# Kernel optimization log

Hardware: AMD Instinct MI355X
Metric: run time of the kernel (lower is better)

## Reference

```python
import jax, jax.numpy as jnp
import numpy as np
from jax import lax

DIM = 256
NUM_HEADS = 8
HEAD_DIM = DIM // NUM_HEADS
SCALE = HEAD_DIM ** -0.5


def _avg_pool(x, k, p):
    # torch AvgPool2d(kernel=k, stride=1, padding=p) with count_include_pad=True
    s = lax.reduce_window(x, 0.0, lax.add,
                          window_dimensions=(1, 1, k, k),
                          window_strides=(1, 1, 1, 1),
                          padding=((0, 0), (0, 0), (p, p), (p, p)))
    return s / (k * k)


def setup_inputs() -> dict:
    key = jax.random.key(0)
    ks = jax.random.split(key, 7)
    x = jax.random.normal(ks[0], (2, DIM, 48, 48), dtype=jnp.float32)
    q_w = jax.random.normal(ks[1], (DIM, DIM), dtype=jnp.float32) * (DIM ** -0.5)
    q_b = jax.random.normal(ks[2], (DIM,), dtype=jnp.float32) * 0.02
    kv_w = jax.random.normal(ks[3], (2 * DIM, DIM), dtype=jnp.float32) * (DIM ** -0.5)
    kv_b = jax.random.normal(ks[4], (2 * DIM,), dtype=jnp.float32) * 0.02
    proj_w = jax.random.normal(ks[5], (DIM, DIM), dtype=jnp.float32) * (DIM ** -0.5)
    proj_b = jax.random.normal(ks[6], (DIM,), dtype=jnp.float32) * 0.02
    return {"x": x, "q_w": q_w, "q_b": q_b, "kv_w": kv_w, "kv_b": kv_b,
            "proj_w": proj_w, "proj_b": proj_b}


def reference(x, q_w, q_b, kv_w, kv_b, proj_w, proj_b):
    B, C, H, W = x.shape
    h, d, N = NUM_HEADS, HEAD_DIM, H * W

    # q = 1x1 conv -> [B, h, N, d]
    q = jnp.einsum('oc,bchw->bohw', q_w, x) + q_b[None, :, None, None]
    q = q.reshape(B, h, d, N).transpose(0, 1, 3, 2)

    # kv is a linear 1x1 conv, so (kv(x)+kv(p1)+kv(p2)+kv(p3))/4 == kv(mean of inputs)
    x_avg = (x + _avg_pool(x, 3, 1) + _avg_pool(x, 5, 2) + _avg_pool(x, 7, 3)) / 4.0
    kv = jnp.einsum('oc,bchw->bohw', kv_w, x_avg) + kv_b[None, :, None, None]
    kv = kv.reshape(B, 2, h, d, N).transpose(1, 0, 2, 4, 3)  # [2, B, h, N, d]
    k, v = kv[0], kv[1]

    attn = jnp.einsum('bhnd,bhmd->bhnm', q, k) * SCALE  # [B, h, N, N]
    attn = jax.nn.softmax(attn, axis=-1)
    y = jnp.einsum('bhnm,bhmd->bhnd', attn, v)  # [B, h, N, d]
    # faithful to torch: transpose(1,2) then flat reshape to [B, C, H, W]
    y = y.transpose(0, 2, 1, 3).reshape(B, C, H, W)

    out = jnp.einsum('oc,bchw->bohw', proj_w, y) + proj_b[None, :, None, None]
    return out
```

## Files before the change

kernel.cpp:

```cpp
#include <hip/hip_runtime.h>
#include <hip/hip_bf16.h>
#include <cstdint>

#define DIMC  256
#define NH    8
#define HD    32
#define NPIX  2304
#define BATCH 2
#define KT    32
#define NT2   (NPIX / KT)

typedef short s16x8 __attribute__((ext_vector_type(8)));
typedef short s16x4 __attribute__((ext_vector_type(4)));
typedef float f32x4 __attribute__((ext_vector_type(4)));

#define MFMA32(A,B,C) __builtin_amdgcn_mfma_f32_16x16x32_bf16(A,B,C,0,0,0)

__device__ inline uint32_t rnau(float x) { return __float_as_uint(x) + 0x8000u; }
__device__ inline uint32_t pk2(uint32_t l_, uint32_t h_) {
  return __builtin_amdgcn_perm(h_, l_, 0x07060302u);
}

__global__ __launch_bounds__(256) void pool_kernel(const float* __restrict__ x,
                                                   float* __restrict__ xavg) {
  const int plane = blockIdx.x;
  const float* xp = x + (size_t)plane * NPIX;
  __shared__ float sx[NPIX];
  __shared__ float h3[NPIX], h5[NPIX], h7[NPIX];
  const int t = threadIdx.x;
#pragma unroll
  for (int r = 0; r < 9; ++r) sx[r * 256 + t] = xp[r * 256 + t];
  __syncthreads();
#pragma unroll
  for (int r = 0; r < 9; ++r) {
    int p = r * 256 + t;
    int i = p / 48, j = p - i * 48;
    float a3 = 0.f, a5 = 0.f, a7 = 0.f;
#pragma unroll
    for (int dj = -3; dj <= 3; ++dj) {
      int jj = j + dj;
      if (jj < 0 || jj >= 48) continue;
      float v = sx[i * 48 + jj];
      a7 += v;
      if (dj >= -2 && dj <= 2) a5 += v;
      if (dj >= -1 && dj <= 1) a3 += v;
    }
    h3[p] = a3; h5[p] = a5; h7[p] = a7;
  }
  __syncthreads();
#pragma unroll
  for (int r = 0; r < 9; ++r) {
    int p = r * 256 + t;
    int i = p / 48, j = p - i * 48;
    float b3 = 0.f, b5 = 0.f, b7 = 0.f;
#pragma unroll
    for (int di = -3; di <= 3; ++di) {
      int ii = i + di;
      if (ii < 0 || ii >= 48) continue;
      int q = ii * 48 + j;
      b7 += h7[q];
      if (di >= -2 && di <= 2) b5 += h5[q];
      if (di >= -1 && di <= 1) b3 += h3[q];
    }
    xavg[(size_t)plane * NPIX + p] =
        0.25f * (sx[p] + b3 * (1.f / 9.f) + b5 * (1.f / 25.f) + b7 * (1.f / 49.f));
  }
}

__global__ __launch_bounds__(256) void conv_all(
    const float* __restrict__ x, const float* __restrict__ xavg,
    const float* __restrict__ qw, const float* __restrict__ kvw,
    const float* __restrict__ pw_,
    short* __restrict__ Xh, short* __restrict__ Ah,
    short* __restrict__ Wth) {
  const int bx = blockIdx.x;
  const int t = threadIdx.x;
  if (bx < 576) {
    const float* src = (bx < 288) ? x : xavg;
    short* dhi = (bx < 288) ? Xh : Ah;
    const int bb = (bx < 288) ? bx : bx - 288;
    const int n0 = (bb % 36) * 64, c0 = ((bb / 36) & 3) * 64, b = bb / 144;
    __shared__ __align__(16) float T[64][68];
    {
      const int c = t >> 2, n4 = (t & 3) * 16;
      const float* sp = src + ((size_t)b * DIMC + c0 + c) * NPIX + n0 + n4;
#pragma unroll
      for (int i2 = 0; i2 < 4; ++i2)
        *(f32x4*)&T[c][n4 + i2 * 4] = *(const f32x4*)(sp + i2 * 4);
    }
    __syncthreads();
    {
      const int n = t >> 2, c4 = (t & 3) * 16;
      float v[16];
#pragma unroll
      for (int i = 0; i < 16; ++i) v[i] = T[c4 + i][n];
      uint32_t a[16];
#pragma unroll
      for (int i = 0; i < 16; ++i) a[i] = rnau(v[i]);
      union { s16x8 s; uint32_t u[4]; } H0, H1;
#pragma unroll
      for (int j = 0; j < 4; ++j) {
        H0.u[j] = pk2(a[2 * j], a[2 * j + 1]);
        H1.u[j] = pk2(a[8 + 2 * j], a[8 + 2 * j + 1]);
      }
      const size_t off = ((size_t)b * NPIX + n0 + n) * DIMC + c0 + c4;
      *(s16x8*)(dhi + off) = H0.s; *(s16x8*)(dhi + off + 8) = H1.s;
    }
  } else {
    const int idx = ((bx - 576) * 256 + t) * 8;
    const float* s;
    int off;
    if (idx < 65536)       { s = qw;  off = idx; }
    else if (idx < 196608) { s = kvw; off = idx - 65536; }
    else                   { s = pw_; off = idx - 196608; }
    f32x4 x0 = *(const f32x4*)(s + off);
    f32x4 x1 = *(const f32x4*)(s + off + 4);
    float v[8] = {x0[0], x0[1], x0[2], x0[3], x1[0], x1[1], x1[2], x1[3]};
    uint32_t a[8];
#pragma unroll
    for (int i = 0; i < 8; ++i) a[i] = rnau(v[i]);
    union { s16x8 s; uint32_t u[4]; } H;
#pragma unroll
    for (int j = 0; j < 4; ++j) H.u[j] = pk2(a[2 * j], a[2 * j + 1]);
    *(s16x8*)(Wth + idx) = H.s;
  }
}

__global__ __launch_bounds__(128) void gemm_qkv_hi(
    const short* __restrict__ Wth,
    const float* __restrict__ q_b, const float* __restrict__ kv_b,
    const short* __restrict__ Xh, const short* __restrict__ Ah,
    short* __restrict__ Qhi, short* __restrict__ Khi, short* __restrict__ Vhi,
    float qscale) {
  __shared__ __align__(16) float Cl[32][68];
  const int by = blockIdx.y;
  const bool isQ = (by < 8);
  const int o0 = isQ ? by * 32 : (by - 8) * 32;
  const short* Wh = isQ ? Wth : Wth + 65536;
  const float* bias = isQ ? q_b : kv_b;
  const short* Inh = isQ ? Xh : Ah;
  const float scale = isQ ? qscale : 1.0f;
  short* d1 = isQ ? Qhi : Khi;
  const int n0 = blockIdx.x * 64;
  const int b  = blockIdx.z;

  const int tid = threadIdx.x;
  const int wave = tid >> 6, lane = tid & 63;
  const int g = lane >> 4, q = lane & 15;

  const short* wph = Wh + ((o0 + wave * 16 + q) * DIMC + g * 8);
  const short* iph = Inh + ((size_t)(b * NPIX + n0 + q) * DIMC + g * 8);

  f32x4 acc[4] = {{0,0,0,0},{0,0,0,0},{0,0,0,0},{0,0,0,0}};
#pragma unroll
  for (int c0 = 0; c0 < DIMC; c0 += 32) {
    s16x8 ah = *(const s16x8*)(wph + c0);
#pragma unroll
    for (int st = 0; st < 4; ++st) {
      s16x8 bh_ = *(const s16x8*)(iph + (size_t)st * 16 * DIMC + c0);
      acc[st] = MFMA32(ah, bh_, acc[st]);
    }
  }
#pragma unroll
  for (int st = 0; st < 4; ++st)
#pragma unroll
    for (int r = 0; r < 4; ++r)
      Cl[wave * 16 + g * 4 + r][st * 16 + q] = acc[st][r];
  __syncthreads();

  if (o0 < 256) {
    const int n = tid >> 1, oq = tid & 1;
    const int h = o0 >> 5;
    const float* bp = bias + o0 + oq * 16;
    float v[16];
#pragma unroll
    for (int i = 0; i < 16; ++i) v[i] = (Cl[oq * 16 + i][n] + bp[i]) * scale;
    uint32_t a[16];
#pragma unroll
    for (int i = 0; i < 16; ++i) a[i] = rnau(v[i]);
    union { s16x8 s; uint32_t u[4]; } H0, H1;
#pragma unroll
    for (int j = 0; j < 4; ++j) {
      H0.u[j] = pk2(a[2 * j], a[2 * j + 1]);
      H1.u[j] = pk2(a[8 + 2 * j], a[8 + 2 * j + 1]);
    }
    const size_t off = ((size_t)((b * 8 + h) * NPIX + n0 + n)) * HD + oq * 16;
    *(s16x8*)(d1 + off) = H0.s; *(s16x8*)(d1 + off + 8) = H1.s;
  } else {
    const int o = tid >> 2, nc = (tid & 3) * 16;
    const int h = (o0 - 256) >> 5;
    const float bv = bias[o0 + o];
    float v[16];
#pragma unroll
    for (int i2 = 0; i2 < 4; ++i2) {
      f32x4 t4 = *(const f32x4*)&Cl[o][nc + i2 * 4];
      v[i2 * 4 + 0] = t4[0] + bv; v[i2 * 4 + 1] = t4[1] + bv;
      v[i2 * 4 + 2] = t4[2] + bv; v[i2 * 4 + 3] = t4[3] + bv;
    }
    uint32_t a[16];
#pragma unroll
    for (int i = 0; i < 16; ++i) a[i] = rnau(v[i]);
    union { s16x8 s; uint32_t u[4]; } H0, H1;
#pragma unroll
    for (int j = 0; j < 4; ++j) {
      H0.u[j] = pk2(a[2 * j], a[2 * j + 1]);
      H1.u[j] = pk2(a[8 + 2 * j], a[8 + 2 * j + 1]);
    }
    const size_t off = ((size_t)((b * 8 + h) * HD + o)) * NPIX + n0 + nc;
    *(s16x8*)(Vhi + off) = H0.s; *(s16x8*)(Vhi + off + 8) = H1.s;
  }
}

__global__ __launch_bounds__(128) void attn_mfma(
    const short* __restrict__ Qhi,
    const short* __restrict__ Khi,
    const short* __restrict__ Vhi,
    short* __restrict__ zh) {
  const int sb = blockIdx.x;
  const int bh = sb / 36;
  const int qb = sb % 36;
  const int tid = threadIdx.x;
  const int wave = tid >> 6, lane = tid & 63;
  const int g = lane >> 4, q = lane & 15;
  const int base = qb * 64 + wave * 32;

  __shared__ __align__(16) short Plds[2][2][16 * 40];
  short* pwA = &Plds[wave][0][0];
  short* pwB = &Plds[wave][1][0];

  const size_t qoff = ((size_t)bh * NPIX + base + q) * HD + g * 8;
  const s16x8 qhA = *(const s16x8*)(Qhi + qoff);
  const s16x8 qhB = *(const s16x8*)(Qhi + qoff + 16 * HD);

  const short* kp = Khi + ((size_t)bh * NPIX + q) * HD + g * 8;
  const short* vp = Vhi + ((size_t)bh * HD + q) * NPIX + g * 8;

  const f32x4 Z4 = {0.f, 0.f, 0.f, 0.f};
  f32x4 OA0 = Z4, OA1 = Z4, OB0 = Z4, OB1 = Z4;
  f32x4 LA = Z4, LB = Z4;
  s16x8 kb[3][2], vb[3][2], pfA, pfB, vp0, vp1;

  union { s16x8 s; uint32_t u[4]; } ONE, ZZ;
  ONE.u[0] = 0x3F803F80u; ONE.u[1] = 0x3F803F80u;
  ONE.u[2] = 0x3F803F80u; ONE.u[3] = 0x3F803F80u;
  ZZ.u[0] = 0; ZZ.u[1] = 0; ZZ.u[2] = 0; ZZ.u[3] = 0;
  const s16x8 ones = ONE.s;
  pfA = ZZ.s; pfB = ZZ.s;
  vp0 = ones; vp1 = ones;

  kb[0][0] = *(const s16x8*)(kp);
  kb[0][1] = *(const s16x8*)(kp + 16 * HD);
  vb[0][0] = *(const s16x8*)(vp);
  vb[0][1] = *(const s16x8*)(vp + 16 * NPIX);
  kb[1][0] = *(const s16x8*)(kp + KT * HD);
  kb[1][1] = *(const s16x8*)(kp + KT * HD + 16 * HD);
  vb[1][0] = *(const s16x8*)(vp + KT);
  vb[1][1] = *(const s16x8*)(vp + KT + 16 * NPIX);

#define ATTN_STEP(CUR, NX2, T)                                                \
  {                                                                           \
    if ((T) + 2 < NT2) {                                                      \
      const short* kpn = kp + ((T) + 2) * (KT * HD);                          \
      const short* vpn = vp + ((T) + 2) * KT;                                 \
      kb[NX2][0] = *(const s16x8*)(kpn);                                      \
      kb[NX2][1] = *(const s16x8*)(kpn + 16 * HD);                            \
      vb[NX2][0] = *(const s16x8*)(vpn);                                      \
      vb[NX2][1] = *(const s16x8*)(vpn + 16 * NPIX);                          \
    }                                                                         \
    f32x4 SA0 = MFMA32(kb[CUR][0], qhA, Z4);                                  \
    f32x4 SA1 = MFMA32(kb[CUR][1], qhA, Z4);                                  \
    f32x4 SB0 = MFMA32(kb[CUR][0], qhB, Z4);                                  \
    f32x4 SB1 = MFMA32(kb[CUR][1], qhB, Z4);                                  \
    OA0 = MFMA32(vp0, pfA, OA0);                                              \
    OA1 = MFMA32(vp1, pfA, OA1);                                              \
    OB0 = MFMA32(vp0, pfB, OB0);                                              \
    OB1 = MFMA32(vp1, pfB, OB1);                                              \
    LA  = MFMA32(ones, pfA, LA);                                              \
    LB  = MFMA32(ones, pfB, LB);                                              \
    {                                                                         \
      f32x4 p0, p1;                                                           \
      p0[0] = exp2f(SA0[0]); p0[1] = exp2f(SA0[1]);                           \
      p0[2] = exp2f(SA0[2]); p0[3] = exp2f(SA0[3]);                           \
      p1[0] = exp2f(SA1[0]); p1[1] = exp2f(SA1[1]);                           \
      p1[2] = exp2f(SA1[2]); p1[3] = exp2f(SA1[3]);                           \
      uint2 w0, w1;                                                           \
      w0.x = pk2(rnau(p0[0]), rnau(p0[1])); w0.y = pk2(rnau(p0[2]), rnau(p0[3])); \
      w1.x = pk2(rnau(p1[0]), rnau(p1[1])); w1.y = pk2(rnau(p1[2]), rnau(p1[3])); \
      *(uint2*)&pwA[q * 40 + g * 4] = w0;                                     \
      *(uint2*)&pwA[q * 40 + 16 + g * 4] = w1;                                \
    }                                                                         \
    {                                                                         \
      f32x4 p0, p1;                                                           \
      p0[0] = exp2f(SB0[0]); p0[1] = exp2f(SB0[1]);                           \
      p0[2] = exp2f(SB0[2]); p0[3] = exp2f(SB0[3]);                           \
      p1[0] = exp2f(SB1[0]); p1[1] = exp2f(SB1[1]);                           \
      p1[2] = exp2f(SB1[2]); p1[3] = exp2f(SB1[3]);                           \
      uint2 w0, w1;                                                           \
      w0.x = pk2(rnau(p0[0]), rnau(p0[1])); w0.y = pk2(rnau(p0[2]), rnau(p0[3])); \
      w1.x = pk2(rnau(p1[0]), rnau(p1[1])); w1.y = pk2(rnau(p1[2]), rnau(p1[3])); \
      *(uint2*)&pwB[q * 40 + g * 4] = w0;                                     \
      *(uint2*)&pwB[q * 40 + 16 + g * 4] = w1;                                \
    }                                                                         \
    vp0 = vb[CUR][0]; vp1 = vb[CUR][1];                                       \
    pfA = *(const s16x8*)&pwA[q * 40 + g * 8];                                \
    pfB = *(const s16x8*)&pwB[q * 40 + g * 8];                                \
  }

#pragma unroll 1
  for (int tt = 0; tt < NT2; tt += 3) {
    ATTN_STEP(0, 2, tt);
    ATTN_STEP(1, 0, tt + 1);
    ATTN_STEP(2, 1, tt + 2);
  }
#undef ATTN_STEP

  OA0 = MFMA32(vp0, pfA, OA0);
  OA1 = MFMA32(vp1, pfA, OA1);
  OB0 = MFMA32(vp0, pfB, OB0);
  OB1 = MFMA32(vp1, pfB, OB1);
  LA  = MFMA32(ones, pfA, LA);
  LB  = MFMA32(ones, pfB, LB);

  const float invA = 1.f / LA[0];
  const float invB = 1.f / LB[0];
  const int h = bh & 7, b = bh >> 3;
  const int nA = base + q, nB = nA + 16;
  {
    const int cA = nA / 9, rA = nA - cA * 9;
    short* zp = zh + ((size_t)(b * NPIX + rA * 256 + h * HD)) * DIMC + cA;
#pragma unroll
    for (int rr = 0; rr < 4; ++rr) {
      zp[(size_t)(g * 4 + rr) * DIMC]      = (short)(rnau(OA0[rr] * invA) >> 16);
      zp[(size_t)(16 + g * 4 + rr) * DIMC] = (short)(rnau(OA1[rr] * invA) >> 16);
    }
  }
  {
    const int cB = nB / 9, rB = nB - cB * 9;
    short* zp = zh + ((size_t)(b * NPIX + rB * 256 + h * HD)) * DIMC + cB;
#pragma unroll
    for (int rr = 0; rr < 4; ++rr) {
      zp[(size_t)(g * 4 + rr) * DIMC]      = (short)(rnau(OB0[rr] * invB) >> 16);
      zp[(size_t)(16 + g * 4 + rr) * DIMC] = (short)(rnau(OB1[rr] * invB) >> 16);
    }
  }
}

__global__ __launch_bounds__(128) void gemm_proj_hi(
    const short* __restrict__ Wh,
    const float* __restrict__ bias,
    const short* __restrict__ Zh,
    float* __restrict__ out) {
  __shared__ __align__(16) float Cl[32][68];
  const int n0 = blockIdx.x * 64;
  const int o0 = blockIdx.y * 32;
  const int b  = blockIdx.z;
  const int tid = threadIdx.x;
  const int wave = tid >> 6, lane = tid & 63;
  const int g = lane >> 4, q = lane & 15;

  const short* wph = Wh + ((o0 + wave * 16 + q) * DIMC + g * 8);
  const short* iph = Zh + ((size_t)(b * NPIX + n0 + q) * DIMC + g * 8);

  f32x4 acc[4] = {{0,0,0,0},{0,0,0,0},{0,0,0,0},{0,0,0,0}};
#pragma unroll
  for (int c0 = 0; c0 < DIMC; c0 += 32) {
    s16x8 ah = *(const s16x8*)(wph + c0);
#pragma unroll
    for (int st = 0; st < 4; ++st) {
      s16x8 bh_ = *(const s16x8*)(iph + (size_t)st * 16 * DIMC + c0);
      acc[st] = MFMA32(ah, bh_, acc[st]);
    }
  }
#pragma unroll
  for (int st = 0; st < 4; ++st)
#pragma unroll
    for (int r = 0; r < 4; ++r)
      Cl[wave * 16 + g * 4 + r][st * 16 + q] = acc[st][r];
  __syncthreads();

  const int o = tid >> 2, nc = (tid & 3) * 16;
  const float bv = bias[o0 + o];
  float* op = out + ((size_t)b * DIMC + o0 + o) * NPIX + n0 + nc;
#pragma unroll
  for (int i2 = 0; i2 < 4; ++i2) {
    f32x4 v = *(const f32x4*)&Cl[o][nc + i2 * 4];
    v[0] += bv; v[1] += bv; v[2] += bv; v[3] += bv;
    *(f32x4*)(op + i2 * 4) = v;
  }
}

extern "C" void kernel_launch(void* const* d_in, const int* in_sizes, int n_in,
                              void* d_out, int out_size, void* d_ws, size_t ws_size,
                              hipStream_t stream) {
  const float* x      = (const float*)d_in[0];
  const float* q_w    = (const float*)d_in[1];
  const float* q_b    = (const float*)d_in[2];
  const float* kv_w   = (const float*)d_in[3];
  const float* kv_b   = (const float*)d_in[4];
  const float* proj_w = (const float*)d_in[5];
  const float* proj_b = (const float*)d_in[6];
  float* out = (float*)d_out;

  char* w = (char*)d_ws;
  float* xavg = (float*)w;
  short* Xh   = (short*)(w + 4718592);
  short* Ah   = (short*)(w + 9437184);
  short* Wth  = (short*)(w + 28311552);
  short* Qhi  = (short*)(w + 29360128);
  short* Khi  = (short*)(w + 31719424);
  short* Vhi  = (short*)(w + 34078720);
  short* Zh   = (short*)(w + 37322752);

  const float qscale = 0.17677669529663689f * 1.4426950408889634f;

  pool_kernel<<<BATCH * DIMC, 256, 0, stream>>>(x, xavg);
  conv_all<<<704, 256, 0, stream>>>(x, xavg, q_w, kv_w, proj_w, Xh, Ah, Wth);
  gemm_qkv_hi<<<dim3(36, 24, 2), 128, 0, stream>>>(Wth, q_b, kv_b,
                                                   Xh, Ah, Qhi, Khi, Vhi, qscale);
  attn_mfma<<<576, 128, 0, stream>>>(Qhi, Khi, Vhi, Zh);
  gemm_proj_hi<<<dim3(36, 8, 2), 128, 0, stream>>>(Wth + 196608, proj_b, Zh, out);
}
```

Before: 165.6 us.

## Split attention key range across four waves with LDS reduction

The attention kernel now gives each block 32 queries and splits the 2304 keys into four 576-key chunks, one per wave. This is a split-K, flash-decoding style partition. Each wave keeps its unnormalized partial outputs and row sums, writes them to shared memory, and the block sums them before normalizing and storing. Without a running max, the exp2 values need no rescaling across chunks. The change doubles the grid and quadruples the waves per query tile to raise occupancy and parallelism on a 256-CU part, at the cost of an extra LDS reduction and more Q loads per key.

```diff
diff --git a/kernel.cpp b/kernel.cpp
--- a/kernel.cpp
+++ b/kernel.cpp
@@ -8,7 +8,8 @@
 #define NPIX  2304
 #define BATCH 2
 #define KT    32
-#define NT2   (NPIX / KT)
+#define NTW   18
+#define KPW   576
 
 typedef short s16x8 __attribute__((ext_vector_type(8)));
 typedef short s16x4 __attribute__((ext_vector_type(4)));
@@ -211,29 +212,30 @@
   }
 }
 
-__global__ __launch_bounds__(128) void attn_mfma(
+__global__ __launch_bounds__(256) void attn_fused(
     const short* __restrict__ Qhi,
     const short* __restrict__ Khi,
     const short* __restrict__ Vhi,
     short* __restrict__ zh) {
-  const int sb = blockIdx.x;
-  const int bh = sb / 36;
-  const int qb = sb % 36;
+  const int blk = blockIdx.x;
+  const int bh = blk / 72;
+  const int qb = blk % 72;
   const int tid = threadIdx.x;
   const int wave = tid >> 6, lane = tid & 63;
   const int g = lane >> 4, q = lane & 15;
-  const int base = qb * 64 + wave * 32;
-
-  __shared__ __align__(16) short Plds[2][2][16 * 40];
-  short* pwA = &Plds[wave][0][0];
-  short* pwB = &Plds[wave][1][0];
+  const int base = qb * 32;
+
+  __shared__ __align__(16) float smemf[4 * 64 * 20];
+  short* pwA = (short*)smemf + wave * 1280;
+  short* pwB = pwA + 640;
+  float (*R)[64][20] = (float (*)[64][20])smemf;
 
   const size_t qoff = ((size_t)bh * NPIX + base + q) * HD + g * 8;
   const s16x8 qhA = *(const s16x8*)(Qhi + qoff);
   const s16x8 qhB = *(const s16x8*)(Qhi + qoff + 16 * HD);
 
-  const short* kp = Khi + ((size_t)bh * NPIX + q) * HD + g * 8;
-  const short* vp = Vhi + ((size_t)bh * HD + q) * NPIX + g * 8;
+  const short* kp = Khi + ((size_t)bh * NPIX + wave * KPW + q) * HD + g * 8;
+  const short* vp = Vhi + ((size_t)bh * HD + q) * NPIX + wave * KPW + g * 8;
 
   const f32x4 Z4 = {0.f, 0.f, 0.f, 0.f};
   f32x4 OA0 = Z4, OA1 = Z4, OB0 = Z4, OB1 = Z4;
@@ -259,7 +261,7 @@
 
 #define ATTN_STEP(CUR, NX2, T)                                                \
   {                                                                           \
-    if ((T) + 2 < NT2) {                                                      \
+    if ((T) + 2 < NTW) {                                                      \
       const short* kpn = kp + ((T) + 2) * (KT * HD);                          \
       const short* vpn = vp + ((T) + 2) * KT;                                 \
       kb[NX2][0] = *(const s16x8*)(kpn);                                      \
@@ -307,7 +309,7 @@
   }
 
 #pragma unroll 1
-  for (int tt = 0; tt < NT2; tt += 3) {
+  for (int tt = 0; tt < NTW; tt += 3) {
     ATTN_STEP(0, 2, tt);
     ATTN_STEP(1, 0, tt + 1);
     ATTN_STEP(2, 1, tt + 2);
@@ -321,27 +323,37 @@
   LA  = MFMA32(ones, pfA, LA);
   LB  = MFMA32(ones, pfB, LB);
 
-  const float invA = 1.f / LA[0];
-  const float invB = 1.f / LB[0];
-  const int h = bh & 7, b = bh >> 3;
-  const int nA = base + q, nB = nA + 16;
+  __syncthreads();
   {
-    const int cA = nA / 9, rA = nA - cA * 9;
-    short* zp = zh + ((size_t)(b * NPIX + rA * 256 + h * HD)) * DIMC + cA;
-#pragma unroll
-    for (int rr = 0; rr < 4; ++rr) {
-      zp[(size_t)(g * 4 + rr) * DIMC]      = (short)(rnau(OA0[rr] * invA) >> 16);
-      zp[(size_t)(16 + g * 4 + rr) * DIMC] = (short)(rnau(OA1[rr] * invA) >> 16);
-    }
-  }
+    float* rw = &R[wave][lane][0];
+    *(f32x4*)&rw[0]  = OA0;
+    *(f32x4*)&rw[4]  = OA1;
+    *(f32x4*)&rw[8]  = OB0;
+    *(f32x4*)&rw[12] = OB1;
+    rw[16] = LA[0];
+    rw[17] = LB[0];
+  }
+  __syncthreads();
   {
-    const int cB = nB / 9, rB = nB - cB * 9;
-    short* zp = zh + ((size_t)(b * NPIX + rB * 256 + h * HD)) * DIMC + cB;
-#pragma unroll
-    for (int rr = 0; rr < 4; ++rr) {
-      zp[(size_t)(g * 4 + rr) * DIMC]      = (short)(rnau(OB0[rr] * invB) >> 16);
-      zp[(size_t)(16 + g * 4 + rr) * DIMC] = (short)(rnau(OB1[rr] * invB) >> 16);
-    }
+    const int l2 = tid & 63, eg = tid >> 6;
+    const int g2 = l2 >> 4, q2 = l2 & 15;
+    f32x4 s = {0.f, 0.f, 0.f, 0.f};
+    float Lt = 0.f;
+#pragma unroll
+    for (int w = 0; w < 4; ++w) {
+      const f32x4 pv = *(const f32x4*)&R[w][l2][eg * 4];
+      s[0] += pv[0]; s[1] += pv[1]; s[2] += pv[2]; s[3] += pv[3];
+      Lt += R[w][l2][16 + (eg >> 1)];
+    }
+    const float inv = 1.f / Lt;
+    const int h = bh & 7, b = bh >> 3;
+    const int n = base + ((eg & 2) ? 16 : 0) + q2;
+    const int d0 = ((eg & 1) ? 16 : 0) + g2 * 4;
+    const int c = n / 9, r = n - c * 9;
+    short* zp = zh + ((size_t)(b * NPIX + r * 256 + h * HD + d0)) * DIMC + c;
+#pragma unroll
+    for (int j = 0; j < 4; ++j)
+      zp[(size_t)j * DIMC] = (short)(rnau(s[j] * inv) >> 16);
   }
 }
 
@@ -417,6 +429,6 @@
   conv_all<<<704, 256, 0, stream>>>(x, xavg, q_w, kv_w, proj_w, Xh, Ah, Wth);
   gemm_qkv_hi<<<dim3(36, 24, 2), 128, 0, stream>>>(Wth, q_b, kv_b,
                                                    Xh, Ah, Qhi, Khi, Vhi, qscale);
-  attn_mfma<<<576, 128, 0, stream>>>(Qhi, Khi, Vhi, Zh);
+  attn_fused<<<1152, 256, 0, stream>>>(Qhi, Khi, Vhi, Zh);
   gemm_proj_hi<<<dim3(36, 8, 2), 128, 0, stream>>>(Wth + 196608, proj_b, Zh, out);
 }
```

Measured after the change: 147.9 us. -10.7%, faster.
